# Kernel tuning notes

Measured on AMD Instinct MI355X. Metric: run time of the kernel, lower is better.

The kernel has to match this reference:

```python
import jax, jax.numpy as jnp
import numpy as np

B, F, A, U = 4096, 64, 8, 32  # batch, n_features, num_att, n_outputs
R = 2.0                       # the 'r' scaling inside exp(kernel * r)


def setup_inputs() -> dict:
    key = jax.random.key(0)
    k1, k2 = jax.random.split(key)
    inputs = jax.random.normal(k1, (B, F), dtype=jnp.float32)
    # per-exclusion-feature attention kernels, stacked: [F, A, F, U]
    limit = float(np.sqrt(6.0 / (F + U)))  # glorot_uniform
    kernels = jax.random.uniform(k2, (F, A, F, U), dtype=jnp.float32,
                                 minval=-limit, maxval=limit)
    return {"inputs": inputs, "kernels": kernels}


def reference(inputs, kernels):
    # inputs: [B, F]; kernels: [j=F excluded-feature index, A, F, U]
    f = inputs.shape[-1]
    mask = 1.0 - jnp.eye(f, dtype=inputs.dtype)          # [j, F]: zero out feature j
    xm = mask[:, None, :] * inputs[None, :, :]           # [j, B, F]
    z = jnp.einsum('jbf,jafu->jabu', xm, kernels)        # [j, A, B, U]
    z = jax.nn.softmax(z, axis=-1)                       # softmax over units
    w = jnp.exp(kernels * R)                             # [j, A, F, U]
    scores = jnp.einsum('jabu,jafu->jabf', z, w)         # [j, A, B, F]
    scores = scores.mean(axis=0)                         # mean over exclusion axis -> [A, B, F]
    return jax.nn.softmax(scores, axis=-1)               # [A, B, F]
```

## Files before the change

### kernel.cpp

```cpp
#include <hip/hip_runtime.h>
#include <hip/hip_bf16.h>
#include <math.h>

#define B_ 4096
#define F_ 64
#define A_ 8
#define U_ 32

typedef float f32x4 __attribute__((ext_vector_type(4)));
typedef short bf16x8 __attribute__((ext_vector_type(8)));

#define KD_OFF (4ull << 20)

static __device__ __forceinline__ unsigned int pk_bf16(float lo, float hi) {
    union { __hip_bfloat162 h2; unsigned int u; } cv;
    cv.h2 = __float22bfloat162_rn(make_float2(lo, hi));
    return cv.u;
}
static __device__ __forceinline__ float rb(float f) {
    unsigned int u = __float_as_uint(f);
    u += 0x7FFFu + ((u >> 16) & 1u);
    return __uint_as_float(u & 0xFFFF0000u);
}

__global__ __launch_bounds__(256) void ife_prep(const float* __restrict__ kern,
                                                unsigned char* __restrict__ ws)
{
    const int bid = blockIdx.x;
    const int a = bid >> 6, j = bid & 63;
    const int t = threadIdx.x;
    __shared__ float st[64][36];

    const float* src = kern + ((size_t)j * A_ + a) * (F_ * U_);
    {
        const int f = t >> 2, u0 = (t & 3) * 8;
        *(float4*)&st[f][u0]     = *(const float4*)&src[f * U_ + u0];
        *(float4*)&st[f][u0 + 4] = *(const float4*)&src[f * U_ + u0 + 4];
    }
    __syncthreads();

    unsigned char* dst = ws + (size_t)bid * 8192;
    const int fragid = t >> 6, lane = t & 63, q = lane >> 4, c = lane & 15;

    {
        const int kc = fragid >> 1, ut = fragid & 1;
        const int f0 = kc * 32 + q * 8, u = ut * 16 + c;
        unsigned int w[4];
        #pragma unroll
        for (int i = 0; i < 4; ++i)
            w[i] = pk_bf16(st[f0 + 2 * i][u], st[f0 + 2 * i + 1][u]);
        *(uint4*)(dst + fragid * 1024 + lane * 16) = make_uint4(w[0], w[1], w[2], w[3]);
    }
    {
        const int f = fragid * 16 + c, u0 = q * 8;
        const float4 wa = *(const float4*)&st[f][u0];
        const float4 wb = *(const float4*)&st[f][u0 + 4];
        unsigned int w[4];
        w[0] = pk_bf16(__expf(2.f * wa.x), __expf(2.f * wa.y));
        w[1] = pk_bf16(__expf(2.f * wa.z), __expf(2.f * wa.w));
        w[2] = pk_bf16(__expf(2.f * wb.x), __expf(2.f * wb.y));
        w[3] = pk_bf16(__expf(2.f * wb.z), __expf(2.f * wb.w));
        *(uint4*)(dst + 4096 + fragid * 1024 + lane * 16) = make_uint4(w[0], w[1], w[2], w[3]);
    }
    if (t < U_)
        ((float*)(ws + KD_OFF))[(size_t)bid * U_ + t] = rb(st[j][t]);
}

__global__ __launch_bounds__(512, 4) void ife_main(const float* __restrict__ x,
                                                   const unsigned char* __restrict__ ws,
                                                   float* __restrict__ out)
{
    const int a = blockIdx.y, bt = blockIdx.x, t = threadIdx.x;
    const int wv = t >> 6, lane = t & 63, q = lane >> 4, c = lane & 15;
    const int grp = wv >> 2, w4 = wv & 3;

    __shared__ __align__(16) float Xf[64][66];
    __shared__ float Kd[64][32];
    __shared__ __align__(16) unsigned int Pbuf[8][16][20];

    bf16x8 Xh[2];
    {
        const float* xr = x + (size_t)(bt * 64 + w4 * 16 + c) * F_;
        #pragma unroll
        for (int kc = 0; kc < 2; ++kc) {
            const float4 va = *(const float4*)&xr[kc * 32 + q * 8];
            const float4 vb = *(const float4*)&xr[kc * 32 + q * 8 + 4];
            union { unsigned int u[4]; bf16x8 v; } H;
            H.u[0] = pk_bf16(va.x, va.y);
            H.u[1] = pk_bf16(va.z, va.w);
            H.u[2] = pk_bf16(vb.x, vb.y);
            H.u[3] = pk_bf16(vb.z, vb.w);
            Xh[kc] = H.v;
        }
    }
    {
        const int row = t >> 3, cb = (t & 7) * 8;
        const float* xsrc = x + (size_t)(bt * 64 + row) * F_ + cb;
        const float4 v0 = *(const float4*)&xsrc[0];
        const float4 v1 = *(const float4*)&xsrc[4];
        Xf[row][cb + 0] = rb(v0.x); Xf[row][cb + 1] = rb(v0.y);
        Xf[row][cb + 2] = rb(v0.z); Xf[row][cb + 3] = rb(v0.w);
        Xf[row][cb + 4] = rb(v1.x); Xf[row][cb + 5] = rb(v1.y);
        Xf[row][cb + 6] = rb(v1.z); Xf[row][cb + 7] = rb(v1.w);
    }
    {
        const float* kd = (const float*)(ws + KD_OFF) + (size_t)a * 64 * U_;
        const int jj = t >> 3, u0 = (t & 7) * 4;
        *(float4*)&Kd[jj][u0] = *(const float4*)&kd[jj * U_ + u0];
    }
    __syncthreads();

    const unsigned int psel = (q < 2) ? 0x05040100u : 0x07060302u;
    const unsigned char* fbase = ws + (size_t)a * 64 * 8192 + (size_t)lane * 16;

    union { unsigned int u[4]; bf16x8 v; } oc;
    oc.u[0] = 0x3F803F80u; oc.u[1] = 0x3F803F80u; oc.u[2] = 0x3F803F80u; oc.u[3] = 0x3F803F80u;
    const bf16x8 ONES = oc.v;
    const f32x4 vzero = (f32x4){0.f, 0.f, 0.f, 0.f};

    f32x4 S0 = vzero, S1 = vzero, S2 = vzero, S3 = vzero;

    const int jb = grp * 32;
    #pragma unroll 1
    for (int jj = 0; jj < 32; ++jj) {
        const int j = jb + jj;

        bf16x8 K[4], W[4];
        {
            const unsigned char* p = fbase + (size_t)j * 8192;
            #pragma unroll
            for (int i = 0; i < 4; ++i) {
                K[i] = *(const bf16x8*)(p + i * 1024);
                W[i] = *(const bf16x8*)(p + 4096 + i * 1024);
            }
        }
        float xj[4];
        #pragma unroll
        for (int r = 0; r < 4; ++r) xj[r] = Xf[w4 * 16 + q * 4 + r][j];
        const float kd0 = Kd[j][c], kd1 = Kd[j][16 + c];

        f32x4 ZA = vzero, ZB = vzero;
        ZA = __builtin_amdgcn_mfma_f32_16x16x32_bf16(Xh[0], K[0], ZA, 0, 0, 0);
        ZA = __builtin_amdgcn_mfma_f32_16x16x32_bf16(Xh[1], K[2], ZA, 0, 0, 0);
        ZB = __builtin_amdgcn_mfma_f32_16x16x32_bf16(Xh[0], K[1], ZB, 0, 0, 0);
        ZB = __builtin_amdgcn_mfma_f32_16x16x32_bf16(Xh[1], K[3], ZB, 0, 0, 0);

        #pragma unroll
        for (int r = 0; r < 4; ++r) {
            const float e0 = __expf(ZA[r] - xj[r] * kd0);
            const float e1 = __expf(ZB[r] - xj[r] * kd1);
            Pbuf[wv][q * 4 + r][c] = pk_bf16(e0, e1);
        }
        asm volatile("s_waitcnt lgkmcnt(0)" ::: "memory");
        const uint4 pa = *(const uint4*)&Pbuf[wv][c][(q & 1) * 8];
        const uint4 pb = *(const uint4*)&Pbuf[wv][c][(q & 1) * 8 + 4];

        union { unsigned int u[4]; bf16x8 v; } E;
        E.u[0] = __builtin_amdgcn_perm(pa.y, pa.x, psel);
        E.u[1] = __builtin_amdgcn_perm(pa.w, pa.z, psel);
        E.u[2] = __builtin_amdgcn_perm(pb.y, pb.x, psel);
        E.u[3] = __builtin_amdgcn_perm(pb.w, pb.z, psel);

        const f32x4 sv = __builtin_amdgcn_mfma_f32_16x16x32_bf16(E.v, ONES, vzero, 0, 0, 0);
        f32x4 D0 = __builtin_amdgcn_mfma_f32_16x16x32_bf16(E.v, W[0], vzero, 0, 0, 0);
        f32x4 D1 = __builtin_amdgcn_mfma_f32_16x16x32_bf16(E.v, W[1], vzero, 0, 0, 0);
        f32x4 D2 = __builtin_amdgcn_mfma_f32_16x16x32_bf16(E.v, W[2], vzero, 0, 0, 0);
        f32x4 D3 = __builtin_amdgcn_mfma_f32_16x16x32_bf16(E.v, W[3], vzero, 0, 0, 0);
        #pragma unroll
        for (int r = 0; r < 4; ++r) {
            const float inv = __builtin_amdgcn_rcpf(sv[r]);
            S0[r] += D0[r] * inv;
            S1[r] += D1[r] * inv;
            S2[r] += D2[r] * inv;
            S3[r] += D3[r] * inv;
        }
    }

    __syncthreads();
    float* Sred = (float*)Xf;
    if (grp == 1) {
        float* p = Sred + (size_t)(w4 * 64 + lane) * 16;
        *(f32x4*)(p + 0)  = S0;
        *(f32x4*)(p + 4)  = S1;
        *(f32x4*)(p + 8)  = S2;
        *(f32x4*)(p + 12) = S3;
    }
    __syncthreads();
    if (grp == 0) {
        const float* p = Sred + (size_t)(w4 * 64 + lane) * 16;
        S0 += *(const f32x4*)(p + 0);
        S1 += *(const f32x4*)(p + 4);
        S2 += *(const f32x4*)(p + 8);
        S3 += *(const f32x4*)(p + 12);

        const float sc = 1.f / 64.f;
        #pragma unroll
        for (int r = 0; r < 4; ++r) {
            const float e0 = __expf(S0[r] * sc);
            const float e1 = __expf(S1[r] * sc);
            const float e2 = __expf(S2[r] * sc);
            const float e3 = __expf(S3[r] * sc);
            float s = e0 + e1 + e2 + e3;
            s += __shfl_xor(s, 1);
            s += __shfl_xor(s, 2);
            s += __shfl_xor(s, 4);
            s += __shfl_xor(s, 8);
            const float inv = 1.f / s;
            const int b = bt * 64 + w4 * 16 + q * 4 + r;
            float* o = out + ((size_t)a * B_ + b) * F_ + c;
            o[0]  = e0 * inv;
            o[16] = e1 * inv;
            o[32] = e2 * inv;
            o[48] = e3 * inv;
        }
    }
}

extern "C" void kernel_launch(void* const* d_in, const int* in_sizes, int n_in,
                              void* d_out, int out_size, void* d_ws, size_t ws_size,
                              hipStream_t stream) {
    (void)in_sizes; (void)n_in; (void)out_size; (void)ws_size;
    const float* x    = (const float*)d_in[0];
    const float* kern = (const float*)d_in[1];
    float* out        = (float*)d_out;
    unsigned char* ws = (unsigned char*)d_ws;

    hipLaunchKernelGGL(ife_prep, dim3(F_ * A_), dim3(256), 0, stream, kern, ws);
    hipLaunchKernelGGL(ife_main, dim3(B_ / 64, A_), dim3(512), 0, stream, x, ws, out);
}
```

Before: 103.6 us.

## Split exclusion axis across all waves, each wave handling all 64 batch rows

Each wave now owns 8 exclusion indices j and processes all four 16-row batch blocks, instead of 4 waves per group sharing 32 j values over a single 16-row block. Each K/W fragment load is reused across four MFMA row blocks, which cuts global/L2 fragment traffic by a factor of four. The cost is far more register state (16 accumulator vectors plus four X fragments), so the occupancy hint drops from 4 to 3 blocks. The final cross-wave reduction becomes an 8-way sum done in four phases through shared memory with extra barriers.

Measured after the change: 109.1 us. 1.05x slower.

```diff
diff --git a/kernel.cpp b/kernel.cpp
--- a/kernel.cpp
+++ b/kernel.cpp
@@ -66,21 +66,21 @@
         ((float*)(ws + KD_OFF))[(size_t)bid * U_ + t] = rb(st[j][t]);
 }
 
-__global__ __launch_bounds__(512, 4) void ife_main(const float* __restrict__ x,
+__global__ __launch_bounds__(512, 3) void ife_main(const float* __restrict__ x,
                                                    const unsigned char* __restrict__ ws,
                                                    float* __restrict__ out)
 {
     const int a = blockIdx.y, bt = blockIdx.x, t = threadIdx.x;
     const int wv = t >> 6, lane = t & 63, q = lane >> 4, c = lane & 15;
-    const int grp = wv >> 2, w4 = wv & 3;
 
     __shared__ __align__(16) float Xf[64][66];
     __shared__ float Kd[64][32];
-    __shared__ __align__(16) unsigned int Pbuf[8][16][20];
-
-    bf16x8 Xh[2];
-    {
-        const float* xr = x + (size_t)(bt * 64 + w4 * 16 + c) * F_;
+    __shared__ __align__(16) unsigned int Pbuf[8][4][16][20];
+
+    bf16x8 Xh[4][2];
+    #pragma unroll
+    for (int rbk = 0; rbk < 4; ++rbk) {
+        const float* xr = x + (size_t)(bt * 64 + rbk * 16 + c) * F_;
         #pragma unroll
         for (int kc = 0; kc < 2; ++kc) {
             const float4 va = *(const float4*)&xr[kc * 32 + q * 8];
@@ -90,7 +90,7 @@
             H.u[1] = pk_bf16(va.z, va.w);
             H.u[2] = pk_bf16(vb.x, vb.y);
             H.u[3] = pk_bf16(vb.z, vb.w);
-            Xh[kc] = H.v;
+            Xh[rbk][kc] = H.v;
         }
     }
     {
@@ -118,95 +118,111 @@
     const bf16x8 ONES = oc.v;
     const f32x4 vzero = (f32x4){0.f, 0.f, 0.f, 0.f};
 
-    f32x4 S0 = vzero, S1 = vzero, S2 = vzero, S3 = vzero;
-
-    const int jb = grp * 32;
+    f32x4 S[4][4];
+    #pragma unroll
+    for (int rbk = 0; rbk < 4; ++rbk) {
+        S[rbk][0] = vzero; S[rbk][1] = vzero; S[rbk][2] = vzero; S[rbk][3] = vzero;
+    }
+
     #pragma unroll 1
-    for (int jj = 0; jj < 32; ++jj) {
-        const int j = jb + jj;
-
-        bf16x8 K[4], W[4];
-        {
-            const unsigned char* p = fbase + (size_t)j * 8192;
+    for (int jj = 0; jj < 8; ++jj) {
+        const int j = (wv << 3) + jj;
+        const unsigned char* p = fbase + (size_t)j * 8192;
+
+        const float kd0 = Kd[j][c], kd1 = Kd[j][16 + c];
+
+        bf16x8 K[4];
+        #pragma unroll
+        for (int i = 0; i < 4; ++i) K[i] = *(const bf16x8*)(p + i * 1024);
+
+        #pragma unroll
+        for (int rbk = 0; rbk < 4; ++rbk) {
+            f32x4 ZA = vzero, ZB = vzero;
+            ZA = __builtin_amdgcn_mfma_f32_16x16x32_bf16(Xh[rbk][0], K[0], ZA, 0, 0, 0);
+            ZA = __builtin_amdgcn_mfma_f32_16x16x32_bf16(Xh[rbk][1], K[2], ZA, 0, 0, 0);
+            ZB = __builtin_amdgcn_mfma_f32_16x16x32_bf16(Xh[rbk][0], K[1], ZB, 0, 0, 0);
+            ZB = __builtin_amdgcn_mfma_f32_16x16x32_bf16(Xh[rbk][1], K[3], ZB, 0, 0, 0);
             #pragma unroll
-            for (int i = 0; i < 4; ++i) {
-                K[i] = *(const bf16x8*)(p + i * 1024);
-                W[i] = *(const bf16x8*)(p + 4096 + i * 1024);
+            for (int r = 0; r < 4; ++r) {
+                const float xj = Xf[rbk * 16 + q * 4 + r][j];
+                const float e0 = __expf(ZA[r] - xj * kd0);
+                const float e1 = __expf(ZB[r] - xj * kd1);
+                Pbuf[wv][rbk][q * 4 + r][c] = pk_bf16(e0, e1);
             }
         }
-        float xj[4];
-        #pragma unroll
-        for (int r = 0; r < 4; ++r) xj[r] = Xf[w4 * 16 + q * 4 + r][j];
-        const float kd0 = Kd[j][c], kd1 = Kd[j][16 + c];
-
-        f32x4 ZA = vzero, ZB = vzero;
-        ZA = __builtin_amdgcn_mfma_f32_16x16x32_bf16(Xh[0], K[0], ZA, 0, 0, 0);
-        ZA = __builtin_amdgcn_mfma_f32_16x16x32_bf16(Xh[1], K[2], ZA, 0, 0, 0);
-        ZB = __builtin_amdgcn_mfma_f32_16x16x32_bf16(Xh[0], K[1], ZB, 0, 0, 0);
-        ZB = __builtin_amdgcn_mfma_f32_16x16x32_bf16(Xh[1], K[3], ZB, 0, 0, 0);
-
+
+        bf16x8 W[4];
+        #pragma unroll
+        for (int i = 0; i < 4; ++i) W[i] = *(const bf16x8*)(p + 4096 + i * 1024);
+
+        asm volatile("s_waitcnt lgkmcnt(0)" ::: "memory");
+
+        #pragma unroll
+        for (int rbk = 0; rbk < 4; ++rbk) {
+            const uint4 pa = *(const uint4*)&Pbuf[wv][rbk][c][(q & 1) * 8];
+            const uint4 pb = *(const uint4*)&Pbuf[wv][rbk][c][(q & 1) * 8 + 4];
+            union { unsigned int u[4]; bf16x8 v; } E;
+            E.u[0] = __builtin_amdgcn_perm(pa.y, pa.x, psel);
+            E.u[1] = __builtin_amdgcn_perm(pa.w, pa.z, psel);
+            E.u[2] = __builtin_amdgcn_perm(pb.y, pb.x, psel);
+            E.u[3] = __builtin_amdgcn_perm(pb.w, pb.z, psel);
+
+            const f32x4 sv = __builtin_amdgcn_mfma_f32_16x16x32_bf16(E.v, ONES, vzero, 0, 0, 0);
+            f32x4 D0 = __builtin_amdgcn_mfma_f32_16x16x32_bf16(E.v, W[0], vzero, 0, 0, 0);
+            f32x4 D1 = __builtin_amdgcn_mfma_f32_16x16x32_bf16(E.v, W[1], vzero, 0, 0, 0);
+            f32x4 D2 = __builtin_amdgcn_mfma_f32_16x16x32_bf16(E.v, W[2], vzero, 0, 0, 0);
+            f32x4 D3 = __builtin_amdgcn_mfma_f32_16x16x32_bf16(E.v, W[3], vzero, 0, 0, 0);
+            #pragma unroll
+            for (int r = 0; r < 4; ++r) {
+                const float inv = __builtin_amdgcn_rcpf(sv[r]);
+                S[rbk][0][r] += D0[r] * inv;
+                S[rbk][1][r] += D1[r] * inv;
+                S[rbk][2][r] += D2[r] * inv;
+                S[rbk][3][r] += D3[r] * inv;
+            }
+        }
+    }
+
+    __syncthreads();
+    float* Sred = (float*)Pbuf;
+    const int si = (wv * 64 + lane) * 20;
+    f32x4 F0 = vzero, F1 = vzero, F2 = vzero, F3 = vzero;
+
+    #pragma unroll
+    for (int ph = 0; ph < 4; ++ph) {
+        *(f32x4*)&Sred[si + 0]  = S[ph][0];
+        *(f32x4*)&Sred[si + 4]  = S[ph][1];
+        *(f32x4*)&Sred[si + 8]  = S[ph][2];
+        *(f32x4*)&Sred[si + 12] = S[ph][3];
+        __syncthreads();
+        if (wv == ph) {
+            #pragma unroll
+            for (int s = 0; s < 8; ++s) {
+                const int b0 = (s * 64 + lane) * 20;
+                F0 += *(const f32x4*)&Sred[b0 + 0];
+                F1 += *(const f32x4*)&Sred[b0 + 4];
+                F2 += *(const f32x4*)&Sred[b0 + 8];
+                F3 += *(const f32x4*)&Sred[b0 + 12];
+            }
+        }
+        __syncthreads();
+    }
+
+    if (wv < 4) {
+        const float sc = 1.f / 64.f;
         #pragma unroll
         for (int r = 0; r < 4; ++r) {
-            const float e0 = __expf(ZA[r] - xj[r] * kd0);
-            const float e1 = __expf(ZB[r] - xj[r] * kd1);
-            Pbuf[wv][q * 4 + r][c] = pk_bf16(e0, e1);
-        }
-        asm volatile("s_waitcnt lgkmcnt(0)" ::: "memory");
-        const uint4 pa = *(const uint4*)&Pbuf[wv][c][(q & 1) * 8];
-        const uint4 pb = *(const uint4*)&Pbuf[wv][c][(q & 1) * 8 + 4];
-
-        union { unsigned int u[4]; bf16x8 v; } E;
-        E.u[0] = __builtin_amdgcn_perm(pa.y, pa.x, psel);
-        E.u[1] = __builtin_amdgcn_perm(pa.w, pa.z, psel);
-        E.u[2] = __builtin_amdgcn_perm(pb.y, pb.x, psel);
-        E.u[3] = __builtin_amdgcn_perm(pb.w, pb.z, psel);
-
-        const f32x4 sv = __builtin_amdgcn_mfma_f32_16x16x32_bf16(E.v, ONES, vzero, 0, 0, 0);
-        f32x4 D0 = __builtin_amdgcn_mfma_f32_16x16x32_bf16(E.v, W[0], vzero, 0, 0, 0);
-        f32x4 D1 = __builtin_amdgcn_mfma_f32_16x16x32_bf16(E.v, W[1], vzero, 0, 0, 0);
-        f32x4 D2 = __builtin_amdgcn_mfma_f32_16x16x32_bf16(E.v, W[2], vzero, 0, 0, 0);
-        f32x4 D3 = __builtin_amdgcn_mfma_f32_16x16x32_bf16(E.v, W[3], vzero, 0, 0, 0);
-        #pragma unroll
-        for (int r = 0; r < 4; ++r) {
-            const float inv = __builtin_amdgcn_rcpf(sv[r]);
-            S0[r] += D0[r] * inv;
-            S1[r] += D1[r] * inv;
-            S2[r] += D2[r] * inv;
-            S3[r] += D3[r] * inv;
-        }
-    }
-
-    __syncthreads();
-    float* Sred = (float*)Xf;
-    if (grp == 1) {
-        float* p = Sred + (size_t)(w4 * 64 + lane) * 16;
-        *(f32x4*)(p + 0)  = S0;
-        *(f32x4*)(p + 4)  = S1;
-        *(f32x4*)(p + 8)  = S2;
-        *(f32x4*)(p + 12) = S3;
-    }
-    __syncthreads();
-    if (grp == 0) {
-        const float* p = Sred + (size_t)(w4 * 64 + lane) * 16;
-        S0 += *(const f32x4*)(p + 0);
-        S1 += *(const f32x4*)(p + 4);
-        S2 += *(const f32x4*)(p + 8);
-        S3 += *(const f32x4*)(p + 12);
-
-        const float sc = 1.f / 64.f;
-        #pragma unroll
-        for (int r = 0; r < 4; ++r) {
-            const float e0 = __expf(S0[r] * sc);
-            const float e1 = __expf(S1[r] * sc);
-            const float e2 = __expf(S2[r] * sc);
-            const float e3 = __expf(S3[r] * sc);
+            const float e0 = __expf(F0[r] * sc);
+            const float e1 = __expf(F1[r] * sc);
+            const float e2 = __expf(F2[r] * sc);
+            const float e3 = __expf(F3[r] * sc);
             float s = e0 + e1 + e2 + e3;
             s += __shfl_xor(s, 1);
             s += __shfl_xor(s, 2);
             s += __shfl_xor(s, 4);
             s += __shfl_xor(s, 8);
             const float inv = 1.f / s;
-            const int b = bt * 64 + w4 * 16 + q * 4 + r;
+            const int b = bt * 64 + wv * 16 + q * 4 + r;
             float* o = out + ((size_t)a * B_ + b) * F_ + c;
             o[0]  = e0 * inv;
             o[16] = e1 * inv;
```

## Swap MFMA operand order to keep softmax in registers, drop LDS transpose

Applied to the files above, without the earlier changes.

The MFMA operands are swapped so the Z accumulator comes out transposed (batch along lanes, units along registers). The exp values can then be packed straight into the B operand of the second MFMA, with no round trip through shared memory and no byte permutes. The softmax denominator is now a register sum plus two cross-lane shuffles instead of an extra MFMA against a ones vector. The exp(2k) fragment layout in prep and the final output softmax are reworked to match: the output uses float4 stores and a shuffle reduction across q groups. The risk is in the layout bookkeeping and in the extra shuffles inside the loop.

Result: faster. 99.97 us (-3.5%).

```diff
diff --git a/kernel.cpp b/kernel.cpp
--- a/kernel.cpp
+++ b/kernel.cpp
@@ -52,9 +52,9 @@
         *(uint4*)(dst + fragid * 1024 + lane * 16) = make_uint4(w[0], w[1], w[2], w[3]);
     }
     {
-        const int f = fragid * 16 + c, u0 = q * 8;
-        const float4 wa = *(const float4*)&st[f][u0];
-        const float4 wb = *(const float4*)&st[f][u0 + 4];
+        const int f = fragid * 16 + c;
+        const float4 wa = *(const float4*)&st[f][q * 4];
+        const float4 wb = *(const float4*)&st[f][16 + q * 4];
         unsigned int w[4];
         w[0] = pk_bf16(__expf(2.f * wa.x), __expf(2.f * wa.y));
         w[1] = pk_bf16(__expf(2.f * wa.z), __expf(2.f * wa.w));
@@ -74,9 +74,9 @@
     const int wv = t >> 6, lane = t & 63, q = lane >> 4, c = lane & 15;
     const int grp = wv >> 2, w4 = wv & 3;
 
-    __shared__ __align__(16) float Xf[64][66];
-    __shared__ float Kd[64][32];
-    __shared__ __align__(16) unsigned int Pbuf[8][16][20];
+    __shared__ __align__(16) float SH[6272];
+    float* Xf = SH;
+    float* Kd = SH + 4224;
 
     bf16x8 Xh[2];
     {
@@ -98,24 +98,18 @@
         const float* xsrc = x + (size_t)(bt * 64 + row) * F_ + cb;
         const float4 v0 = *(const float4*)&xsrc[0];
         const float4 v1 = *(const float4*)&xsrc[4];
-        Xf[row][cb + 0] = rb(v0.x); Xf[row][cb + 1] = rb(v0.y);
-        Xf[row][cb + 2] = rb(v0.z); Xf[row][cb + 3] = rb(v0.w);
-        Xf[row][cb + 4] = rb(v1.x); Xf[row][cb + 5] = rb(v1.y);
-        Xf[row][cb + 6] = rb(v1.z); Xf[row][cb + 7] = rb(v1.w);
+        float* xd = Xf + row * 66 + cb;
+        xd[0] = rb(v0.x); xd[1] = rb(v0.y); xd[2] = rb(v0.z); xd[3] = rb(v0.w);
+        xd[4] = rb(v1.x); xd[5] = rb(v1.y); xd[6] = rb(v1.z); xd[7] = rb(v1.w);
     }
     {
         const float* kd = (const float*)(ws + KD_OFF) + (size_t)a * 64 * U_;
         const int jj = t >> 3, u0 = (t & 7) * 4;
-        *(float4*)&Kd[jj][u0] = *(const float4*)&kd[jj * U_ + u0];
-    }
-    __syncthreads();
-
-    const unsigned int psel = (q < 2) ? 0x05040100u : 0x07060302u;
+        *(float4*)&Kd[jj * 32 + u0] = *(const float4*)&kd[jj * U_ + u0];
+    }
+    __syncthreads();
+
     const unsigned char* fbase = ws + (size_t)a * 64 * 8192 + (size_t)lane * 16;
-
-    union { unsigned int u[4]; bf16x8 v; } oc;
-    oc.u[0] = 0x3F803F80u; oc.u[1] = 0x3F803F80u; oc.u[2] = 0x3F803F80u; oc.u[3] = 0x3F803F80u;
-    const bf16x8 ONES = oc.v;
     const f32x4 vzero = (f32x4){0.f, 0.f, 0.f, 0.f};
 
     f32x4 S0 = vzero, S1 = vzero, S2 = vzero, S3 = vzero;
@@ -124,51 +118,56 @@
     #pragma unroll 1
     for (int jj = 0; jj < 32; ++jj) {
         const int j = jb + jj;
-
-        bf16x8 K[4], W[4];
-        {
-            const unsigned char* p = fbase + (size_t)j * 8192;
-            #pragma unroll
-            for (int i = 0; i < 4; ++i) {
-                K[i] = *(const bf16x8*)(p + i * 1024);
-                W[i] = *(const bf16x8*)(p + 4096 + i * 1024);
-            }
-        }
-        float xj[4];
-        #pragma unroll
-        for (int r = 0; r < 4; ++r) xj[r] = Xf[w4 * 16 + q * 4 + r][j];
-        const float kd0 = Kd[j][c], kd1 = Kd[j][16 + c];
+        const unsigned char* p = fbase + (size_t)j * 8192;
+
+        const bf16x8 K0 = *(const bf16x8*)(p + 0);
+        const bf16x8 K1 = *(const bf16x8*)(p + 1024);
+        const bf16x8 K2 = *(const bf16x8*)(p + 2048);
+        const bf16x8 K3 = *(const bf16x8*)(p + 3072);
+        const bf16x8 W0 = *(const bf16x8*)(p + 4096);
+        const bf16x8 W1 = *(const bf16x8*)(p + 5120);
+        const bf16x8 W2 = *(const bf16x8*)(p + 6144);
+        const bf16x8 W3 = *(const bf16x8*)(p + 7168);
+
+        const float xj = Xf[(w4 * 16 + c) * 66 + j];
+        const f32x4 kda = *(const f32x4*)&Kd[j * 32 + q * 4];
+        const f32x4 kdb = *(const f32x4*)&Kd[j * 32 + 16 + q * 4];
 
         f32x4 ZA = vzero, ZB = vzero;
-        ZA = __builtin_amdgcn_mfma_f32_16x16x32_bf16(Xh[0], K[0], ZA, 0, 0, 0);
-        ZA = __builtin_amdgcn_mfma_f32_16x16x32_bf16(Xh[1], K[2], ZA, 0, 0, 0);
-        ZB = __builtin_amdgcn_mfma_f32_16x16x32_bf16(Xh[0], K[1], ZB, 0, 0, 0);
-        ZB = __builtin_amdgcn_mfma_f32_16x16x32_bf16(Xh[1], K[3], ZB, 0, 0, 0);
-
+        ZA = __builtin_amdgcn_mfma_f32_16x16x32_bf16(K0, Xh[0], ZA, 0, 0, 0);
+        ZA = __builtin_amdgcn_mfma_f32_16x16x32_bf16(K2, Xh[1], ZA, 0, 0, 0);
+        ZB = __builtin_amdgcn_mfma_f32_16x16x32_bf16(K1, Xh[0], ZB, 0, 0, 0);
+        ZB = __builtin_amdgcn_mfma_f32_16x16x32_bf16(K3, Xh[1], ZB, 0, 0, 0);
+
+        float eA[4], eB[4];
         #pragma unroll
         for (int r = 0; r < 4; ++r) {
-            const float e0 = __expf(ZA[r] - xj[r] * kd0);
-            const float e1 = __expf(ZB[r] - xj[r] * kd1);
-            Pbuf[wv][q * 4 + r][c] = pk_bf16(e0, e1);
-        }
-        asm volatile("s_waitcnt lgkmcnt(0)" ::: "memory");
-        const uint4 pa = *(const uint4*)&Pbuf[wv][c][(q & 1) * 8];
-        const uint4 pb = *(const uint4*)&Pbuf[wv][c][(q & 1) * 8 + 4];
-
+            eA[r] = __expf(ZA[r] - xj * kda[r]);
+            eB[r] = __expf(ZB[r] - xj * kdb[r]);
+        }
         union { unsigned int u[4]; bf16x8 v; } E;
-        E.u[0] = __builtin_amdgcn_perm(pa.y, pa.x, psel);
-        E.u[1] = __builtin_amdgcn_perm(pa.w, pa.z, psel);
-        E.u[2] = __builtin_amdgcn_perm(pb.y, pb.x, psel);
-        E.u[3] = __builtin_amdgcn_perm(pb.w, pb.z, psel);
-
-        const f32x4 sv = __builtin_amdgcn_mfma_f32_16x16x32_bf16(E.v, ONES, vzero, 0, 0, 0);
-        f32x4 D0 = __builtin_amdgcn_mfma_f32_16x16x32_bf16(E.v, W[0], vzero, 0, 0, 0);
-        f32x4 D1 = __builtin_amdgcn_mfma_f32_16x16x32_bf16(E.v, W[1], vzero, 0, 0, 0);
-        f32x4 D2 = __builtin_amdgcn_mfma_f32_16x16x32_bf16(E.v, W[2], vzero, 0, 0, 0);
-        f32x4 D3 = __builtin_amdgcn_mfma_f32_16x16x32_bf16(E.v, W[3], vzero, 0, 0, 0);
+        E.u[0] = pk_bf16(eA[0], eA[1]);
+        E.u[1] = pk_bf16(eA[2], eA[3]);
+        E.u[2] = pk_bf16(eB[0], eB[1]);
+        E.u[3] = pk_bf16(eB[2], eB[3]);
+
+        float s = 0.f;
+        #pragma unroll
+        for (int i = 0; i < 4; ++i) {
+            const float lo = __uint_as_float(E.u[i] << 16);
+            const float hi = __uint_as_float(E.u[i] & 0xFFFF0000u);
+            s += lo + hi;
+        }
+        s += __shfl_xor(s, 16, 64);
+        s += __shfl_xor(s, 32, 64);
+        const float inv = __builtin_amdgcn_rcpf(s);
+
+        const f32x4 D0 = __builtin_amdgcn_mfma_f32_16x16x32_bf16(W0, E.v, vzero, 0, 0, 0);
+        const f32x4 D1 = __builtin_amdgcn_mfma_f32_16x16x32_bf16(W1, E.v, vzero, 0, 0, 0);
+        const f32x4 D2 = __builtin_amdgcn_mfma_f32_16x16x32_bf16(W2, E.v, vzero, 0, 0, 0);
+        const f32x4 D3 = __builtin_amdgcn_mfma_f32_16x16x32_bf16(W3, E.v, vzero, 0, 0, 0);
         #pragma unroll
         for (int r = 0; r < 4; ++r) {
-            const float inv = __builtin_amdgcn_rcpf(sv[r]);
             S0[r] += D0[r] * inv;
             S1[r] += D1[r] * inv;
             S2[r] += D2[r] * inv;
@@ -177,41 +176,47 @@
     }
 
     __syncthreads();
-    float* Sred = (float*)Xf;
+    float* Sred = SH;
     if (grp == 1) {
-        float* p = Sred + (size_t)(w4 * 64 + lane) * 16;
-        *(f32x4*)(p + 0)  = S0;
-        *(f32x4*)(p + 4)  = S1;
-        *(f32x4*)(p + 8)  = S2;
-        *(f32x4*)(p + 12) = S3;
+        float* pp = Sred + (size_t)(w4 * 64 + lane) * 20;
+        *(f32x4*)(pp + 0)  = S0;
+        *(f32x4*)(pp + 4)  = S1;
+        *(f32x4*)(pp + 8)  = S2;
+        *(f32x4*)(pp + 12) = S3;
     }
     __syncthreads();
     if (grp == 0) {
-        const float* p = Sred + (size_t)(w4 * 64 + lane) * 16;
-        S0 += *(const f32x4*)(p + 0);
-        S1 += *(const f32x4*)(p + 4);
-        S2 += *(const f32x4*)(p + 8);
-        S3 += *(const f32x4*)(p + 12);
+        const float* pp = Sred + (size_t)(w4 * 64 + lane) * 20;
+        S0 += *(const f32x4*)(pp + 0);
+        S1 += *(const f32x4*)(pp + 4);
+        S2 += *(const f32x4*)(pp + 8);
+        S3 += *(const f32x4*)(pp + 12);
 
         const float sc = 1.f / 64.f;
+        float ex[4][4];
+        float part = 0.f;
         #pragma unroll
         for (int r = 0; r < 4; ++r) {
-            const float e0 = __expf(S0[r] * sc);
-            const float e1 = __expf(S1[r] * sc);
-            const float e2 = __expf(S2[r] * sc);
-            const float e3 = __expf(S3[r] * sc);
-            float s = e0 + e1 + e2 + e3;
-            s += __shfl_xor(s, 1);
-            s += __shfl_xor(s, 2);
-            s += __shfl_xor(s, 4);
-            s += __shfl_xor(s, 8);
-            const float inv = 1.f / s;
-            const int b = bt * 64 + w4 * 16 + q * 4 + r;
-            float* o = out + ((size_t)a * B_ + b) * F_ + c;
-            o[0]  = e0 * inv;
-            o[16] = e1 * inv;
-            o[32] = e2 * inv;
-            o[48] = e3 * inv;
+            ex[0][r] = __expf(S0[r] * sc);
+            ex[1][r] = __expf(S1[r] * sc);
+            ex[2][r] = __expf(S2[r] * sc);
+            ex[3][r] = __expf(S3[r] * sc);
+            part += ex[0][r] + ex[1][r] + ex[2][r] + ex[3][r];
+        }
+        part += __shfl_xor(part, 16, 64);
+        part += __shfl_xor(part, 32, 64);
+        const float inv = 1.f / part;
+
+        const int b = bt * 64 + w4 * 16 + c;
+        float* o = out + ((size_t)a * B_ + b) * F_;
+        #pragma unroll
+        for (int ft = 0; ft < 4; ++ft) {
+            float4 v;
+            v.x = ex[ft][0] * inv;
+            v.y = ex[ft][1] * inv;
+            v.z = ex[ft][2] * inv;
+            v.w = ex[ft][3] * inv;
+            *(float4*)&o[ft * 16 + q * 4] = v;
         }
     }
 }
```
